# Kernel optimization log

Measured on AMD Instinct MI355X. Metric: run time of the kernel, lower is better.

## Reference

```python
import jax, jax.numpy as jnp
import numpy as np

NUM_HEADS = 8

def setup_inputs() -> dict:
    key = jax.random.key(0)
    ks = jax.random.split(key, 10)
    B, S, D = 4, 2048, 512
    scale = 1.0 / np.sqrt(D)
    return {
        "x": jax.random.normal(ks[0], (B, S, D), dtype=jnp.float32),
        "q": jax.random.normal(ks[1], (B, S, D), dtype=jnp.float32),
        "Wq": jax.random.normal(ks[2], (D, D), dtype=jnp.float32) * scale,
        "bq": jax.random.normal(ks[3], (D,), dtype=jnp.float32) * 0.01,
        "Wk": jax.random.normal(ks[4], (D, D), dtype=jnp.float32) * scale,
        "bk": jax.random.normal(ks[5], (D,), dtype=jnp.float32) * 0.01,
        "Wv": jax.random.normal(ks[6], (D, D), dtype=jnp.float32) * scale,
        "bv": jax.random.normal(ks[7], (D,), dtype=jnp.float32) * 0.01,
        "Wo": jax.random.normal(ks[8], (D, D), dtype=jnp.float32) * scale,
        "bo": jax.random.normal(ks[9], (D,), dtype=jnp.float32) * 0.01,
    }

def reference(x, q, Wq, bq, Wk, bk, Wv, bv, Wo, bo):
    B, S, D = x.shape
    H = NUM_HEADS
    Dh = D // H
    # Linear layers: y = x @ W.T + b (torch nn.Linear convention)
    def split_heads(t):  # [B,S,D] -> [B,H,S,Dh]
        return t.reshape(B, -1, H, Dh).transpose(0, 2, 1, 3)
    Q = split_heads(q @ Wq.T + bq)
    K = split_heads(x @ Wk.T + bk)
    V = split_heads(x @ Wv.T + bv)
    logits = jnp.einsum('bhqd,bhkd->bhqk', Q, K) / jnp.sqrt(jnp.asarray(Dh, Q.dtype))
    attn = jax.nn.softmax(logits, axis=-1)
    out = jnp.einsum('bhqk,bhkd->bhqd', attn, V)  # [B,H,S,Dh]
    concat = out.transpose(0, 2, 1, 3).reshape(B, -1, D)
    return concat @ Wo.T + bo
```

## Files before the change

### kernel.cpp

```cpp
#include <hip/hip_runtime.h>
#include <stdint.h>

typedef __bf16 bf16_t;
typedef bf16_t bf16x8 __attribute__((ext_vector_type(8)));
typedef bf16_t bf16x4 __attribute__((ext_vector_type(4)));
typedef bf16_t bf16x2 __attribute__((ext_vector_type(2)));
typedef float f32x4 __attribute__((ext_vector_type(4)));
typedef float f32x16 __attribute__((ext_vector_type(16)));
typedef uint32_t u32x4 __attribute__((ext_vector_type(4)));

#define DEV __device__ __forceinline__

DEV void gload_lds16(const void* g, void* l) {
  __builtin_amdgcn_global_load_lds(
      (__attribute__((address_space(1))) void*)(g),
      (__attribute__((address_space(3))) void*)(l), 16, 0, 0);
}

__global__ __launch_bounds__(256) void cvt_all_kernel(
    const float* __restrict__ x, const float* __restrict__ q,
    const float* __restrict__ Wq, const float* __restrict__ Wk,
    const float* __restrict__ Wv, const float* __restrict__ Wo,
    bf16_t* __restrict__ xb, bf16_t* __restrict__ qb, bf16_t* __restrict__ Wb) {
  const int y = blockIdx.y;
  int i = blockIdx.x * 256 + threadIdx.x;
  const float* s;
  bf16_t* d;
  if (y == 0) { s = x; d = xb; }
  else if (y == 1) { s = q; d = qb; }
  else {
    if (i >= 131072) return;
    int widx = i >> 15;
    s = (widx == 0) ? Wq : (widx == 1) ? Wk : (widx == 2) ? Wv : Wo;
    d = Wb + (size_t)widx * 262144;
    i &= 32767;
  }
  const float4* sp = (const float4*)s + (size_t)i * 2;
  float4 a = sp[0], b = sp[1];
  bf16x8 o;
  o[0] = (bf16_t)a.x; o[1] = (bf16_t)a.y; o[2] = (bf16_t)a.z; o[3] = (bf16_t)a.w;
  o[4] = (bf16_t)b.x; o[5] = (bf16_t)b.y; o[6] = (bf16_t)b.z; o[7] = (bf16_t)b.w;
  *(bf16x8*)(d + (size_t)i * 8) = o;
}

DEV void gemm_core(const bf16_t* __restrict__ A, const bf16_t* __restrict__ W,
                   char* smem, f32x4 (&acc)[4][4]) {
  const int tid = threadIdx.x;
  const int lane = tid & 63;
  const int wid = tid >> 6;
  const int wr = wid >> 1, wc = wid & 1;
  const int bx = blockIdx.x, by = blockIdx.y;

  uint32_t goffA[4], goffB[4], ldsoff[4];
#pragma unroll
  for (int c = 0; c < 4; ++c) {
    uint32_t o = (uint32_t)wid * 4096u + (uint32_t)c * 1024u + (uint32_t)lane * 16u;
    uint32_t row = o >> 7;
    uint32_t inner = (o & 127u) ^ ((row & 7u) << 4);
    goffA[c] = ((uint32_t)by * 128u + row) * 1024u + inner;
    goffB[c] = ((uint32_t)bx * 128u + row) * 1024u + inner;
    ldsoff[c] = o - (uint32_t)lane * 16u;
  }
  uint32_t offA[4][2], offB[4][2];
#pragma unroll
  for (int i = 0; i < 4; ++i)
#pragma unroll
    for (int kk = 0; kk < 2; ++kk) {
      uint32_t ra = (uint32_t)(wr * 64 + i * 16 + (lane & 15));
      offA[i][kk] = ra * 128u + (((uint32_t)kk * 64u + ((lane >> 4) * 16u)) ^ ((ra & 7u) << 4));
      uint32_t rb = (uint32_t)(wc * 64 + i * 16 + (lane & 15));
      offB[i][kk] = rb * 128u + (((uint32_t)kk * 64u + ((lane >> 4) * 16u)) ^ ((rb & 7u) << 4));
    }

  const char* Ab = (const char*)A;
  const char* Wb = (const char*)W;

#pragma unroll
  for (int c = 0; c < 4; ++c) {
    gload_lds16(Ab + goffA[c], smem + ldsoff[c]);
    gload_lds16(Wb + goffB[c], smem + 16384 + ldsoff[c]);
  }
  asm volatile("s_waitcnt vmcnt(0)" ::: "memory");
  __syncthreads();

#pragma unroll 1
  for (int kt = 0; kt < 8; ++kt) {
    const int buf = kt & 1;
    char* cur = smem + buf * 32768;
    if (kt < 7) {
      char* nxt = smem + (buf ^ 1) * 32768;
      uint32_t gk = (uint32_t)(kt + 1) * 128u;
#pragma unroll
      for (int c = 0; c < 4; ++c) {
        gload_lds16(Ab + goffA[c] + gk, nxt + ldsoff[c]);
        gload_lds16(Wb + goffB[c] + gk, nxt + 16384 + ldsoff[c]);
      }
    }
    bf16x8 af[4][2], bfr[4][2];
#pragma unroll
    for (int kk = 0; kk < 2; ++kk)
#pragma unroll
      for (int i = 0; i < 4; ++i) {
        af[i][kk] = *(const bf16x8*)(cur + offA[i][kk]);
        bfr[i][kk] = *(const bf16x8*)(cur + 16384 + offB[i][kk]);
      }
    __builtin_amdgcn_s_setprio(1);
#pragma unroll
    for (int kk = 0; kk < 2; ++kk)
#pragma unroll
      for (int mi = 0; mi < 4; ++mi)
#pragma unroll
        for (int nj = 0; nj < 4; ++nj)
          acc[mi][nj] = __builtin_amdgcn_mfma_f32_16x16x32_bf16(
              af[mi][kk], bfr[nj][kk], acc[mi][nj], 0, 0, 0);
    __builtin_amdgcn_s_setprio(0);
    asm volatile("s_waitcnt vmcnt(0)" ::: "memory");
    __syncthreads();
  }
}

__global__ __launch_bounds__(256) void gemm_qkv_kernel(
    const bf16_t* __restrict__ xb, const bf16_t* __restrict__ qb,
    const bf16_t* __restrict__ Wb, const float* __restrict__ bq,
    const float* __restrict__ bk, const float* __restrict__ bv,
    bf16_t* __restrict__ Qh, bf16_t* __restrict__ Kh, bf16_t* __restrict__ VT) {
  __shared__ char smem[65536];
  const int z = blockIdx.z;
  const bf16_t* A = (z == 0) ? qb : xb;
  const bf16_t* W = Wb + (size_t)z * 262144;
  const float* bias = (z == 0) ? bq : (z == 1) ? bk : bv;

  f32x4 acc[4][4] = {};
  gemm_core(A, W, smem, acc);

  const int lane = threadIdx.x & 63, wid = threadIdx.x >> 6;
  const int wr = wid >> 1, wc = wid & 1;
  const int colbase = blockIdx.x * 128 + wc * 64 + (lane & 15);
  const int rowbase = blockIdx.y * 128 + wr * 64 + ((lane >> 4) << 2);

  if (z == 2) {
#pragma unroll
    for (int nj = 0; nj < 4; ++nj) {
      int c = colbase + nj * 16;
      float bb = bias[c];
      int h = c >> 6, d = c & 63;
#pragma unroll
      for (int mi = 0; mi < 4; ++mi) {
        int r0 = rowbase + mi * 16;
        int b = r0 >> 11, s0 = r0 & 2047;
        bf16x4 v;
#pragma unroll
        for (int rr = 0; rr < 4; ++rr) v[rr] = (bf16_t)(acc[mi][nj][rr] + bb);
        *(bf16x4*)(VT + ((size_t)((b << 3) | h) * 64 + d) * 2048 + s0) = v;
      }
    }
  } else {
    bf16_t* O = (z == 0) ? Qh : Kh;
    const float scl = (z == 0) ? 0.18033688f : 1.0f;
#pragma unroll
    for (int nj = 0; nj < 4; ++nj) {
      int c = colbase + nj * 16;
      float bb = bias[c];
      int h = c >> 6, d = c & 63;
#pragma unroll
      for (int mi = 0; mi < 4; ++mi)
#pragma unroll
        for (int rr = 0; rr < 4; ++rr) {
          int r = rowbase + mi * 16 + rr;
          int b = r >> 11, s = r & 2047;
          O[((size_t)((b << 3) | h) * 2048 + s) * 64 + d] = (bf16_t)((acc[mi][nj][rr] + bb) * scl);
        }
    }
  }
}

__global__ __launch_bounds__(256) void gemm_out_kernel(
    const bf16_t* __restrict__ ctx, const bf16_t* __restrict__ Wo,
    const float* __restrict__ bo, float* __restrict__ out) {
  __shared__ char smem[65536];
  f32x4 acc[4][4] = {};
  gemm_core(ctx, Wo, smem, acc);

  const int lane = threadIdx.x & 63, wid = threadIdx.x >> 6;
  const int wr = wid >> 1, wc = wid & 1;
  const int colbase = blockIdx.x * 128 + wc * 64 + (lane & 15);
  const int rowbase = blockIdx.y * 128 + wr * 64 + ((lane >> 4) << 2);
#pragma unroll
  for (int nj = 0; nj < 4; ++nj) {
    int c = colbase + nj * 16;
    float bb = bo[c];
#pragma unroll
    for (int mi = 0; mi < 4; ++mi)
#pragma unroll
      for (int rr = 0; rr < 4; ++rr) {
        int r = rowbase + mi * 16 + rr;
        out[(size_t)r * 512 + c] = acc[mi][nj][rr] + bb;
      }
  }
}

__global__ __launch_bounds__(256, 2) void attn_kernel(
    const bf16_t* __restrict__ Qh, const bf16_t* __restrict__ Kh,
    const bf16_t* __restrict__ VT, bf16_t* __restrict__ ctx) {
  __shared__ char smem[32768];
  char* Kb = smem;
  char* Vb = smem + 16384;
  const int tid = threadIdx.x, lane = tid & 63, wid = tid >> 6;
  const int l31 = lane & 31, h = lane >> 5;
  const int bid = blockIdx.x + 16 * blockIdx.y;
  const int qt = (bid >> 3) & 15;
  const int bh = (bid & 7) * 4 + (bid >> 7);

  const char* Kbase = (const char*)Kh + (size_t)bh * 262144;
  const char* Vbase = (const char*)VT + (size_t)bh * 262144;
  const char* Qbase = (const char*)Qh + (size_t)bh * 262144;

  const int qrow = qt * 128 + wid * 32 + l31;
  bf16x8 qf[4];
#pragma unroll
  for (int ks = 0; ks < 4; ++ks)
    qf[ks] = *(const bf16x8*)(Qbase + (size_t)qrow * 128 + ks * 32 + h * 16);

  uint32_t kgo[2], vgo[2], lo[2];
#pragma unroll
  for (int c = 0; c < 2; ++c) {
    uint32_t o = (uint32_t)c * 4096u + (uint32_t)wid * 1024u + (uint32_t)lane * 16u;
    uint32_t rowp = o >> 8;
    uint32_t innp = (o & 255u) ^ ((rowp & 15u) << 4);
    kgo[c] = (o & ~255u) + innp;
    vgo[c] = (2u * rowp + (innp >> 7)) * 4096u + (innp & 127u);
    lo[c] = o - (uint32_t)lane * 16u;
  }

  const uint32_t swz = (uint32_t)(l31 >> 1) << 4;
  uint32_t fbase[2], fcol[4];
#pragma unroll
  for (int c = 0; c < 2; ++c) fbase[c] = (uint32_t)(16 * c + (l31 >> 1)) * 256u;
#pragma unroll
  for (int ks = 0; ks < 4; ++ks)
    fcol[ks] = ((uint32_t)((l31 & 1) * 128 + ks * 32 + h * 16)) ^ swz;

  f32x16 oacc[2] = {};
  float m_run = 0.0f, l_part = 0.f;

#pragma unroll
  for (int c = 0; c < 2; ++c) {
    gload_lds16(Kbase + kgo[c], Kb + lo[c]);
    gload_lds16(Vbase + vgo[c], Vb + lo[c]);
  }
  asm volatile("s_waitcnt vmcnt(0)" ::: "memory");
  __syncthreads();

#pragma unroll 1
  for (int t = 0; t < 32; ++t) {
    const uint32_t cur = ((uint32_t)t & 1u) << 13;
    if (t < 31) {
      const uint32_t nxt = cur ^ 8192u;
      const char* Kn = Kbase + (size_t)(t + 1) * 8192;
      const char* Vn = Vbase + (size_t)(t + 1) * 128;
#pragma unroll
      for (int c = 0; c < 2; ++c) {
        gload_lds16(Kn + kgo[c], Kb + nxt + lo[c]);
        gload_lds16(Vn + vgo[c], Vb + nxt + lo[c]);
      }
    }

    f32x16 sT[2] = {};
#pragma unroll
    for (int c = 0; c < 2; ++c) {
      __builtin_amdgcn_s_setprio(1);
#pragma unroll
      for (int ks = 0; ks < 4; ++ks) {
        bf16x8 kf = *(const bf16x8*)(Kb + cur + fbase[c] + fcol[ks]);
        sT[c] = __builtin_amdgcn_mfma_f32_32x32x16_bf16(kf, qf[ks], sT[c], 0, 0, 0);
      }
      __builtin_amdgcn_s_setprio(0);
    }

    uint32_t cw[2][8];
    float la0 = 0.f, la1 = 0.f, la2 = 0.f, la3 = 0.f;
#pragma unroll
    for (int c = 0; c < 2; ++c)
#pragma unroll
      for (int w = 0; w < 8; ++w) {
        float p0 = __builtin_exp2f(sT[c][2 * w] - m_run);
        float p1 = __builtin_exp2f(sT[c][2 * w + 1] - m_run);
        if ((w & 3) == 0) la0 += p0 + p1;
        else if ((w & 3) == 1) la1 += p0 + p1;
        else if ((w & 3) == 2) la2 += p0 + p1;
        else la3 += p0 + p1;
        bf16x2 tp; tp[0] = (bf16_t)p0; tp[1] = (bf16_t)p1;
        cw[c][w] = __builtin_bit_cast(uint32_t, tp);
      }
    float ladd = (la0 + la1) + (la2 + la3);
    if (!__all(ladd <= 16384.0f)) {
      float mx = sT[0][0];
#pragma unroll
      for (int c = 0; c < 2; ++c)
#pragma unroll
        for (int r = 0; r < 16; ++r) mx = fmaxf(mx, sT[c][r]);
      mx = fmaxf(mx, __shfl_xor(mx, 32));
      float mnew = fmaxf(m_run, mx);
      float sc = __builtin_exp2f(m_run - mnew);
      l_part *= sc;
#pragma unroll
      for (int r = 0; r < 16; ++r) { oacc[0][r] *= sc; oacc[1][r] *= sc; }
      m_run = mnew;
      la0 = la1 = la2 = la3 = 0.f;
#pragma unroll
      for (int c = 0; c < 2; ++c)
#pragma unroll
        for (int w = 0; w < 8; ++w) {
          float p0 = __builtin_exp2f(sT[c][2 * w] - m_run);
          float p1 = __builtin_exp2f(sT[c][2 * w + 1] - m_run);
          if ((w & 3) == 0) la0 += p0 + p1;
          else if ((w & 3) == 1) la1 += p0 + p1;
          else if ((w & 3) == 2) la2 += p0 + p1;
          else la3 += p0 + p1;
          bf16x2 tp; tp[0] = (bf16_t)p0; tp[1] = (bf16_t)p1;
          cw[c][w] = __builtin_bit_cast(uint32_t, tp);
        }
      ladd = (la0 + la1) + (la2 + la3);
    }
    l_part += ladd;

    bf16x8 pa[4];
#pragma unroll
    for (int s = 0; s < 4; ++s) {
      const int c = s >> 1, sp = s & 1;
      uint32_t w0 = cw[c][4 * sp + 0], w1 = cw[c][4 * sp + 1];
      uint32_t w2 = cw[c][4 * sp + 2], w3 = cw[c][4 * sp + 3];
      uint32_t snd0 = h ? w0 : w2;
      uint32_t snd1 = h ? w1 : w3;
      uint32_t rcv0 = (uint32_t)__shfl_xor((int)snd0, 32);
      uint32_t rcv1 = (uint32_t)__shfl_xor((int)snd1, 32);
      u32x4 ta;
      ta[0] = h ? rcv0 : w0;
      ta[1] = h ? rcv1 : w1;
      ta[2] = h ? w2 : rcv0;
      ta[3] = h ? w3 : rcv1;
      pa[s] = __builtin_bit_cast(bf16x8, ta);
    }

#pragma unroll
    for (int dc = 0; dc < 2; ++dc) {
      __builtin_amdgcn_s_setprio(1);
#pragma unroll
      for (int ks = 0; ks < 4; ++ks) {
        bf16x8 vf = *(const bf16x8*)(Vb + cur + fbase[dc] + fcol[ks]);
        oacc[dc] = __builtin_amdgcn_mfma_f32_32x32x16_bf16(vf, pa[ks], oacc[dc], 0, 0, 0);
      }
      __builtin_amdgcn_s_setprio(0);
    }

    asm volatile("s_waitcnt vmcnt(0)" ::: "memory");
    __syncthreads();
  }

  float l = l_part + __shfl_xor(l_part, 32);
  float inv = 1.0f / l;
  const int b = bh >> 3, hh = bh & 7;
  bf16_t* crow = ctx + ((size_t)(b * 2048 + qrow)) * 512 + hh * 64;
#pragma unroll
  for (int dc = 0; dc < 2; ++dc)
#pragma unroll
    for (int m = 0; m < 4; ++m) {
      bf16x4 v;
#pragma unroll
      for (int r = 0; r < 4; ++r) v[r] = (bf16_t)(oacc[dc][4 * m + r] * inv);
      *(bf16x4*)(crow + dc * 32 + m * 8 + h * 4) = v;
    }
}

extern "C" void kernel_launch(void* const* d_in, const int* in_sizes, int n_in,
                              void* d_out, int out_size, void* d_ws, size_t ws_size,
                              hipStream_t stream) {
  const float* x  = (const float*)d_in[0];
  const float* q  = (const float*)d_in[1];
  const float* Wq = (const float*)d_in[2];
  const float* bq = (const float*)d_in[3];
  const float* Wk = (const float*)d_in[4];
  const float* bk = (const float*)d_in[5];
  const float* Wv = (const float*)d_in[6];
  const float* bv = (const float*)d_in[7];
  const float* Wo = (const float*)d_in[8];
  const float* bo = (const float*)d_in[9];

  char* ws = (char*)d_ws;
  bf16_t* xb  = (bf16_t*)(ws + 0);
  bf16_t* qb  = (bf16_t*)(ws + 8388608);
  bf16_t* Wb  = (bf16_t*)(ws + 16777216);
  bf16_t* Qh  = (bf16_t*)(ws + 18874368);
  bf16_t* Kh  = (bf16_t*)(ws + 27262976);
  bf16_t* VT  = (bf16_t*)(ws + 35651584);
  bf16_t* ctx = (bf16_t*)(ws + 44040192);

  cvt_all_kernel<<<dim3(2048, 3), 256, 0, stream>>>(x, q, Wq, Wk, Wv, Wo, xb, qb, Wb);
  gemm_qkv_kernel<<<dim3(4, 64, 3), 256, 0, stream>>>(xb, qb, Wb, bq, bk, bv, Qh, Kh, VT);
  attn_kernel<<<dim3(16, 32), 256, 0, stream>>>(Qh, Kh, VT, ctx);
  gemm_out_kernel<<<dim3(4, 64), 256, 0, stream>>>(ctx, Wb + 3 * 262144, bo, (float*)d_out);
}
```

Before: 116.8 us.

## Split attention KV sequence across two wave groups and merge partial softmax states

Doubles the attention block to 512 threads, with two groups of four waves each processing half of the key/value tiles for the same 128 query rows. Each group has its own double-buffered K/V LDS region, and at the end the second group writes its partial accumulators, running max and sum to LDS so the first group can do a flash-style rescale and merge. This aims to raise the number of waves working on the attention loop, since the grid has only 512 blocks, at the cost of doubled LDS per block and a merge step through shared memory.

```diff
diff --git a/kernel.cpp b/kernel.cpp
--- a/kernel.cpp
+++ b/kernel.cpp
@@ -199,13 +199,12 @@
   }
 }
 
-__global__ __launch_bounds__(256, 2) void attn_kernel(
+__global__ __launch_bounds__(512, 4) void attn_kernel(
     const bf16_t* __restrict__ Qh, const bf16_t* __restrict__ Kh,
     const bf16_t* __restrict__ VT, bf16_t* __restrict__ ctx) {
-  __shared__ char smem[32768];
-  char* Kb = smem;
-  char* Vb = smem + 16384;
+  __shared__ char smem[65536];
   const int tid = threadIdx.x, lane = tid & 63, wid = tid >> 6;
+  const int wq = wid & 3, half = wid >> 2;
   const int l31 = lane & 31, h = lane >> 5;
   const int bid = blockIdx.x + 16 * blockIdx.y;
   const int qt = (bid >> 3) & 15;
@@ -215,7 +214,10 @@
   const char* Vbase = (const char*)VT + (size_t)bh * 262144;
   const char* Qbase = (const char*)Qh + (size_t)bh * 262144;
 
-  const int qrow = qt * 128 + wid * 32 + l31;
+  char* Kb = smem + half * 16384;
+  char* Vb = smem + 32768 + half * 16384;
+
+  const int qrow = qt * 128 + wq * 32 + l31;
   bf16x8 qf[4];
 #pragma unroll
   for (int ks = 0; ks < 4; ++ks)
@@ -224,7 +226,7 @@
   uint32_t kgo[2], vgo[2], lo[2];
 #pragma unroll
   for (int c = 0; c < 2; ++c) {
-    uint32_t o = (uint32_t)c * 4096u + (uint32_t)wid * 1024u + (uint32_t)lane * 16u;
+    uint32_t o = (uint32_t)c * 4096u + (uint32_t)wq * 1024u + (uint32_t)lane * 16u;
     uint32_t rowp = o >> 8;
     uint32_t innp = (o & 255u) ^ ((rowp & 15u) << 4);
     kgo[c] = (o & ~255u) + innp;
@@ -243,21 +245,26 @@
   f32x16 oacc[2] = {};
   float m_run = 0.0f, l_part = 0.f;
 
-#pragma unroll
-  for (int c = 0; c < 2; ++c) {
-    gload_lds16(Kbase + kgo[c], Kb + lo[c]);
-    gload_lds16(Vbase + vgo[c], Vb + lo[c]);
+  {
+    const char* K0 = Kbase + (size_t)(half * 16) * 8192;
+    const char* V0 = Vbase + (size_t)(half * 16) * 128;
+#pragma unroll
+    for (int c = 0; c < 2; ++c) {
+      gload_lds16(K0 + kgo[c], Kb + lo[c]);
+      gload_lds16(V0 + vgo[c], Vb + lo[c]);
+    }
   }
   asm volatile("s_waitcnt vmcnt(0)" ::: "memory");
   __syncthreads();
 
 #pragma unroll 1
-  for (int t = 0; t < 32; ++t) {
+  for (int t = 0; t < 16; ++t) {
+    const int tt = half * 16 + t;
     const uint32_t cur = ((uint32_t)t & 1u) << 13;
-    if (t < 31) {
+    if (t < 15) {
       const uint32_t nxt = cur ^ 8192u;
-      const char* Kn = Kbase + (size_t)(t + 1) * 8192;
-      const char* Vn = Vbase + (size_t)(t + 1) * 128;
+      const char* Kn = Kbase + (size_t)(tt + 1) * 8192;
+      const char* Vn = Vbase + (size_t)(tt + 1) * 128;
 #pragma unroll
       for (int c = 0; c < 2; ++c) {
         gload_lds16(Kn + kgo[c], Kb + nxt + lo[c]);
@@ -357,19 +364,42 @@
     __syncthreads();
   }
 
-  float l = l_part + __shfl_xor(l_part, 32);
-  float inv = 1.0f / l;
-  const int b = bh >> 3, hh = bh & 7;
-  bf16_t* crow = ctx + ((size_t)(b * 2048 + qrow)) * 512 + hh * 64;
-#pragma unroll
-  for (int dc = 0; dc < 2; ++dc)
-#pragma unroll
-    for (int m = 0; m < 4; ++m) {
-      bf16x4 v;
-#pragma unroll
-      for (int r = 0; r < 4; ++r) v[r] = (bf16_t)(oacc[dc][4 * m + r] * inv);
-      *(bf16x4*)(crow + dc * 32 + m * 8 + h * 4) = v;
-    }
+  float l_red = l_part + __shfl_xor(l_part, 32);
+
+  if (half == 1) {
+    char* pb = smem + (uint32_t)wq * 9216u + (uint32_t)lane * 144u;
+    *(f32x16*)(pb) = oacc[0];
+    *(f32x16*)(pb + 64) = oacc[1];
+    *(float*)(pb + 128) = m_run;
+    *(float*)(pb + 132) = l_red;
+  }
+  __syncthreads();
+  if (half == 0) {
+    const char* pb = smem + (uint32_t)wq * 9216u + (uint32_t)lane * 144u;
+    f32x16 o1a = *(const f32x16*)(pb);
+    f32x16 o1b = *(const f32x16*)(pb + 64);
+    float m1 = *(const float*)(pb + 128);
+    float l1 = *(const float*)(pb + 132);
+    float mmax = fmaxf(m_run, m1);
+    float a0 = __builtin_exp2f(m_run - mmax);
+    float a1 = __builtin_exp2f(m1 - mmax);
+    float inv = 1.0f / (a0 * l_red + a1 * l1);
+    float s0 = a0 * inv, s1 = a1 * inv;
+    const int b = bh >> 3, hh = bh & 7;
+    bf16_t* crow = ctx + ((size_t)(b * 2048 + qrow)) * 512 + hh * 64;
+#pragma unroll
+    for (int dc = 0; dc < 2; ++dc) {
+      const f32x16 o1 = dc ? o1b : o1a;
+#pragma unroll
+      for (int m = 0; m < 4; ++m) {
+        bf16x4 v;
+#pragma unroll
+        for (int r = 0; r < 4; ++r)
+          v[r] = (bf16_t)(oacc[dc][4 * m + r] * s0 + o1[4 * m + r] * s1);
+        *(bf16x4*)(crow + dc * 32 + m * 8 + h * 4) = v;
+      }
+    }
+  }
 }
 
 extern "C" void kernel_launch(void* const* d_in, const int* in_sizes, int n_in,
@@ -397,6 +427,6 @@
 
   cvt_all_kernel<<<dim3(2048, 3), 256, 0, stream>>>(x, q, Wq, Wk, Wv, Wo, xb, qb, Wb);
   gemm_qkv_kernel<<<dim3(4, 64, 3), 256, 0, stream>>>(xb, qb, Wb, bq, bk, bv, Qh, Kh, VT);
-  attn_kernel<<<dim3(16, 32), 256, 0, stream>>>(Qh, Kh, VT, ctx);
+  attn_kernel<<<dim3(16, 32), 512, 0, stream>>>(Qh, Kh, VT, ctx);
   gemm_out_kernel<<<dim3(4, 64), 256, 0, stream>>>(ctx, Wb + 3 * 262144, bo, (float*)d_out);
 }
```

Measured after the change: 266.5 us. 128% more time.
